# Optimization experiments

Hardware: AMD Instinct MI355X
Metric: run time of the kernel (lower is better)

The kernel has to match this reference:

```python
import jax, jax.numpy as jnp
import numpy as np

N_POI, EMBED, N_EDGES, N_LAYERS, N_HEADS = 50000, 128, 800000, 2, 4
B, L = 512, 64  # sessions, session length (equal-length sections)


def setup_inputs() -> dict:
    key = jax.random.key(0)
    ks = jax.random.split(key, 12)
    d = EMBED
    return {
        "poi_embeds": jax.random.normal(ks[0], (N_POI, d), jnp.float32),
        "dist_edges": jax.random.randint(ks[1], (2, N_EDGES), 0, N_POI),
        "dist_vec": jax.random.uniform(ks[2], (N_EDGES,), jnp.float32),
        "data_poi": jax.random.randint(ks[3], (B,), 0, N_POI),
        "data_x": jax.random.randint(ks[4], (B * L,), 0, N_POI),
        "lin_w": jax.random.normal(ks[5], (N_LAYERS, d, d), jnp.float32) / np.sqrt(d),
        "lin_b": jnp.zeros((N_LAYERS, d), jnp.float32),
        "in_proj_w": jax.random.normal(ks[6], (3 * d, d), jnp.float32) / np.sqrt(d),
        "in_proj_b": jnp.zeros((3 * d,), jnp.float32),
        "out_proj_w": jax.random.normal(ks[7], (d, d), jnp.float32) / np.sqrt(d),
        "out_proj_b": jnp.zeros((d,), jnp.float32),
    }


def reference(poi_embeds, dist_edges, dist_vec, data_poi, data_x,
              lin_w, lin_b, in_proj_w, in_proj_b, out_proj_w, out_proj_b):
    n_poi, d = poi_embeds.shape
    # --- edge augmentation done in GeoGraph.__init__: reversed edges + self loops ---
    loop = jnp.arange(n_poi)
    edges = jnp.concatenate([dist_edges, dist_edges[::-1], jnp.stack([loop, loop])], axis=1)
    dvec = jnp.concatenate([dist_vec, dist_vec, jnp.zeros((n_poi,), dist_vec.dtype)])
    src, dst = edges[0], edges[1]
    # degree of source nodes (torch_geometric.utils.degree on nodes1)
    deg = jnp.zeros((n_poi,), poi_embeds.dtype).at[src].add(1.0)
    w = jax.lax.rsqrt(deg[src] * deg[dst]) * jnp.exp(-dvec ** 2)  # [E]

    enc = poi_embeds
    for i in range(lin_w.shape[0]):
        h = enc @ lin_w[i].T + lin_b[i]                              # [N, d]
        msg = w[:, None] * h[dst]                                    # [E, d] gather
        agg = jax.ops.segment_sum(msg, src, num_segments=n_poi)      # [N, d] scatter
        agg = jnp.where(agg >= 0, agg, 0.01 * agg)                   # leaky_relu(0.01)
        enc = agg / jnp.maximum(jnp.linalg.norm(agg, axis=-1, keepdims=True), 1e-12)

    tar_embed = enc[data_poi]                                        # [B, d]
    seq = enc[data_x].reshape(B, L, d)                               # padded sessions

    # --- nn.MultiheadAttention (batch_first) ---
    hd = d // N_HEADS
    qkv = seq @ in_proj_w.T + in_proj_b                              # [B, L, 3d]
    q, k, v = jnp.split(qkv, 3, axis=-1)
    heads = lambda t: t.reshape(B, L, N_HEADS, hd).transpose(0, 2, 1, 3)
    q, k, v = heads(q), heads(k), heads(v)
    scores = jnp.einsum('bhqd,bhkd->bhqk', q, k) / np.sqrt(hd)
    attn = jax.nn.softmax(scores, axis=-1)
    o = jnp.einsum('bhqk,bhkd->bhqd', attn, v).transpose(0, 2, 1, 3).reshape(B, L, d)
    o = o @ out_proj_w.T + out_proj_b

    aggr_feat = o.mean(axis=1)                                       # mean over padded length
    return aggr_feat, tar_embed
```

## Files before the change

### kernel.cpp

```cpp
#include <hip/hip_runtime.h>
#include <hip/hip_fp16.h>

#define NPOI 50000
#define EMB 128
#define NEDGE 800000
#define EAUG (2 * NEDGE + NPOI)
#define BATCH 512
#define SEQL 64
#define NHEADS 4
#define HDIM 32
#define NB 196
#define P1_BLOCKS ((NEDGE + 2047) / 2048)
#define SLAB_CAP 10240
#define BUCKET_CAP 10240

typedef _Float16 half8 __attribute__((ext_vector_type(8)));
typedef _Float16 half4 __attribute__((ext_vector_type(4)));
typedef _Float16 half2t __attribute__((ext_vector_type(2)));
typedef float f32x4 __attribute__((ext_vector_type(4)));
typedef unsigned long long u64;

union HBits { _Float16 h; unsigned short u; };


#define N4_POI (NPOI * 128 / 4)
#define N4_LIN (2 * 128 * 128 / 4)
#define N4_INW (384 * 128 / 4)
#define CVT_TOT (N4_POI + N4_LIN + N4_INW + NB)

__global__ void cvt_all_kernel(const float* __restrict__ poi, const float* __restrict__ linw,
                               const float* __restrict__ inw,
                               _Float16* __restrict__ poi_h, _Float16* __restrict__ linw_h,
                               _Float16* __restrict__ inw_h, int* __restrict__ bcur) {
    int i = blockIdx.x * blockDim.x + threadIdx.x;
    const float* src; _Float16* dst; int j = i;
    if (i < N4_POI) { src = poi; dst = poi_h; }
    else if (i < N4_POI + N4_LIN) { j = i - N4_POI; src = linw; dst = linw_h; }
    else if (i < N4_POI + N4_LIN + N4_INW) { j = i - N4_POI - N4_LIN; src = inw; dst = inw_h; }
    else if (i < CVT_TOT) { int b = i - (N4_POI + N4_LIN + N4_INW); bcur[b] = b * SLAB_CAP; return; }
    else return;
    float4 v = ((const float4*)src)[j];
    half4 h = { (_Float16)v.x, (_Float16)v.y, (_Float16)v.z, (_Float16)v.w };
    ((half4*)dst)[j] = h;
}


__global__ __launch_bounds__(256) void partition_kernel(
    const int* __restrict__ e0, const int* __restrict__ e1,
    const float* __restrict__ dv, int* __restrict__ bcur,
    u64* __restrict__ staging)
{
    __shared__ u64 stg[4096];
    __shared__ int lh[NB], lbase[NB], gb[NB];
    __shared__ int sc[256];
    const int t = threadIdx.x;
    const int blockBase = blockIdx.x * 2048;
    for (int j = t; j < NB; j += 256) lh[j] = 0;
    __syncthreads();

    u64 vals[16];
    unsigned br[16];
#pragma unroll
    for (int i = 0; i < 8; ++i) {
        br[2 * i] = 0xFFFFFFFFu;
        br[2 * i + 1] = 0xFFFFFFFFu;
        int g = blockBase + i * 256 + t;
        if (g < NEDGE) {
            int s = e0[g], d = e1[g];
            unsigned db = __float_as_uint(dv[g]);
            vals[2 * i]     = ((u64)s << 48) | ((u64)d << 32) | db;
            vals[2 * i + 1] = ((u64)d << 48) | ((u64)s << 32) | db;
            int bs = s >> 8, bd = d >> 8;
            int rs = atomicAdd(&lh[bs], 1);
            int rd_ = atomicAdd(&lh[bd], 1);
            br[2 * i]     = ((unsigned)bs << 16) | (unsigned)rs;
            br[2 * i + 1] = ((unsigned)bd << 16) | (unsigned)rd_;
        }
    }
    __syncthreads();
    sc[t] = (t < NB) ? lh[t] : 0;
    __syncthreads();
    for (int o = 1; o < 256; o <<= 1) {
        int u = (t >= o) ? sc[t - o] : 0;
        __syncthreads();
        sc[t] += u;
        __syncthreads();
    }
    if (t < NB) {
        lbase[t] = sc[t] - lh[t];
        gb[t] = (lh[t] > 0) ? atomicAdd(&bcur[t], lh[t]) : 0;
    }
    __syncthreads();
#pragma unroll
    for (int i = 0; i < 16; ++i) {
        if (br[i] != 0xFFFFFFFFu) {
            int b = br[i] >> 16, r = br[i] & 0xFFFF;
            stg[lbase[b] + r] = vals[i];
        }
    }
    __syncthreads();
    const int total = sc[255];
    for (int j = t; j < total; j += 256) {
        u64 v = stg[j];
        int b = (int)(v >> 56);
        staging[(size_t)gb[b] + (unsigned)(j - lbase[b])] = v;
    }
}


__global__ __launch_bounds__(256) void hist_kernel(const u64* __restrict__ staging,
                                                   const int* __restrict__ bcur,
                                                   float* __restrict__ rd,
                                                   int* __restrict__ bsum) {
    __shared__ int cnt[256];
    __shared__ int red[256];
    const int b = blockIdx.x, t = threadIdx.x;
    cnt[t] = 0;
    __syncthreads();
    const int base = b * SLAB_CAP;
    const int n = bcur[b] - base;
    for (int j = t; j < n; j += 256)
        atomicAdd(&cnt[(int)(staging[base + j] >> 48) & 255], 1);
    __syncthreads();
    int node = b * 256 + t;
    int rowsz = 0;
    if (node < NPOI) {
        rowsz = cnt[t] + 1;
        rd[node] = rsqrtf((float)rowsz);
    }
    red[t] = rowsz;
    __syncthreads();
    for (int o = 128; o > 0; o >>= 1) {
        if (t < o) red[t] += red[t + o];
        __syncthreads();
    }
    if (t == 0) bsum[b] = red[0];
}


__global__ __launch_bounds__(256) void csr_sort_kernel(
    const u64* __restrict__ staging, const int* __restrict__ bcur,
    const int* __restrict__ bsum, const float* __restrict__ rd,
    int* __restrict__ offs, unsigned* __restrict__ ew)
{
    const int k = blockIdx.x;
    const int node0 = k * 256;
    __shared__ unsigned outb[BUCKET_CAP];
    __shared__ int cnt[256], base2[256];
    __shared__ float rdl[256];
    __shared__ int bb_sh;
    const int t = threadIdx.x;
    const int node = node0 + t;
    cnt[t] = 0;
    rdl[t] = (node < NPOI) ? rd[node] : 0.f;
    {
        int partial = 0;
        for (int j = t; j < k; j += 256) partial += bsum[j];
        base2[t] = partial;
        __syncthreads();
        for (int o = 128; o > 0; o >>= 1) {
            if (t < o) base2[t] += base2[t + o];
            __syncthreads();
        }
        if (t == 0) bb_sh = base2[0];
        __syncthreads();
    }
    const int bucketbase = bb_sh;
    __syncthreads();
    const int sb = k * SLAB_CAP;
    const int n = bcur[k] - sb;
    for (int j = t; j < n; j += 256)
        atomicAdd(&cnt[(int)(staging[sb + j] >> 48) & 255], 1);
    __syncthreads();
    int rowsz = (node < NPOI) ? cnt[t] + 1 : 0;
    base2[t] = rowsz;
    __syncthreads();
    for (int o = 1; o < 256; o <<= 1) {
        int u = (t >= o) ? base2[t - o] : 0;
        __syncthreads();
        base2[t] += u;
        __syncthreads();
    }
    int myexc = base2[t] - rowsz;
    __syncthreads();
    base2[t] = myexc;
    cnt[t] = 0;
    if (node < NPOI) {
        offs[node] = bucketbase + myexc;
        if (node == NPOI - 1) offs[NPOI] = bucketbase + myexc + rowsz;
    }
    __syncthreads();
    for (int j = t; j < n; j += 256) {
        u64 e = staging[sb + j];
        int sl = (int)(e >> 48) & 255;
        int d = (int)(e >> 32) & 0xFFFF;
        float dist = __uint_as_float((unsigned)e);
        float w = rdl[sl] * rd[d] * expf(-dist * dist);
        HBits cv; cv.h = (_Float16)w;
        int r = atomicAdd(&cnt[sl], 1);
        outb[base2[sl] + r] = ((unsigned)d << 16) | cv.u;
    }
    __syncthreads();
    if (node < NPOI) {
        float w = rdl[t] * rdl[t];
        HBits cv; cv.h = (_Float16)w;
        outb[base2[t] + cnt[t]] = ((unsigned)node << 16) | cv.u;
    }
    __syncthreads();
    const int ntot = (node0 + 256 < NPOI ? n + 256 : n + (NPOI - node0));
    for (int j = t; j < ntot; j += 256) ew[bucketbase + j] = outb[j];
}


__global__ __launch_bounds__(256) void gemm_mfma_f16(
    const _Float16* __restrict__ A, const int* __restrict__ gidx,
    const _Float16* __restrict__ B, const float* __restrict__ bias,
    _Float16* __restrict__ C, int M, int N)
{
    __shared__ _Float16 Asl[64][136];
    __shared__ _Float16 Bsl[64][136];
    const int tid = threadIdx.x;
    const int n0 = blockIdx.x * 64;
    const int m0 = blockIdx.y * 64;

#pragma unroll
    for (int i = 0; i < 4; ++i) {
        int u = i * 256 + tid;
        int r = u >> 4;
        int c = u & 15;
        int row = m0 + r;
        int ar = (row < M) ? (gidx ? gidx[row] : row) : 0;
        *(float4*)&Asl[r][c * 8] = *(const float4*)(A + (size_t)ar * 128 + c * 8);
        *(float4*)&Bsl[r][c * 8] = *(const float4*)(B + (size_t)(n0 + r) * 128 + c * 8);
    }
    __syncthreads();

    const int wave = tid >> 6;
    const int lane = tid & 63;
    const int l15 = lane & 15;
    const int quad = lane >> 4;

    f32x4 acc[4];
#pragma unroll
    for (int mt = 0; mt < 4; ++mt) acc[mt] = (f32x4){0.f, 0.f, 0.f, 0.f};

#pragma unroll
    for (int ks = 0; ks < 4; ++ks) {
        half8 bfrag = *(const half8*)&Bsl[wave * 16 + l15][quad * 8 + ks * 32];
#pragma unroll
        for (int mt = 0; mt < 4; ++mt) {
            half8 afrag = *(const half8*)&Asl[mt * 16 + l15][quad * 8 + ks * 32];
            acc[mt] = __builtin_amdgcn_mfma_f32_16x16x32_f16(afrag, bfrag, acc[mt], 0, 0, 0);
        }
    }

    const int col = wave * 16 + l15;
    const float bv = bias[n0 + col];
    __syncthreads();
#pragma unroll
    for (int mt = 0; mt < 4; ++mt)
#pragma unroll
        for (int r = 0; r < 4; ++r)
            Asl[mt * 16 + quad * 4 + r][col] = (_Float16)(acc[mt][r] + bv);
    __syncthreads();
#pragma unroll
    for (int i = 0; i < 2; ++i) {
        int u = i * 256 + tid;
        int r = u >> 3;
        int c = u & 7;
        int m = m0 + r;
        if (m < M)
            *(half8*)(C + (size_t)m * N + n0 + c * 8) = *(const half8*)&Asl[r][c * 8];
    }
}


__global__ __launch_bounds__(64) void aggregate_kernel(
    const _Float16* __restrict__ h, const int* __restrict__ offs,
    const unsigned* __restrict__ ew, float* __restrict__ enc_out,
    _Float16* __restrict__ enc_h)
{
    const int row = blockIdx.x;
    const int lane = threadIdx.x;
    const int beg = offs[row];
    const int end = offs[row + 1];
    float ax = 0.f, ay = 0.f;
#pragma unroll 8
    for (int e = beg; e < end; ++e) {
        unsigned p = ew[e];
        HBits cv; cv.u = (unsigned short)(p & 0xffffu);
        float w = (float)cv.h;
        int d = p >> 16;
        half2t hv = *(const half2t*)(h + (size_t)d * 128 + lane * 2);
        ax += w * (float)hv[0];
        ay += w * (float)hv[1];
    }
    ax = ax >= 0.f ? ax : 0.01f * ax;
    ay = ay >= 0.f ? ay : 0.01f * ay;
    float ss = ax * ax + ay * ay;
#pragma unroll
    for (int o = 32; o > 0; o >>= 1) ss += __shfl_xor(ss, o);
    float inv = 1.f / fmaxf(sqrtf(ss), 1e-12f);
    float ex = ax * inv, ey = ay * inv;
    *(float2*)(enc_out + (size_t)row * 128 + lane * 2) = make_float2(ex, ey);
    half2t hv = { (_Float16)ex, (_Float16)ey };
    *(half2t*)(enc_h + (size_t)row * 128 + lane * 2) = hv;
}


__global__ __launch_bounds__(256) void attn_mfma_kernel(
    const _Float16* __restrict__ qkv, const float* __restrict__ outw,
    const float* __restrict__ outb, const float* __restrict__ enc,
    const int* __restrict__ data_poi, float* __restrict__ out)
{
    const int b = blockIdx.x;
    const int wave = threadIdx.x >> 6;
    const int lane = threadIdx.x & 63;
    const int l15 = lane & 15;
    const int quad = lane >> 4;
    __shared__ _Float16 pP[NHEADS][64][72];
    __shared__ _Float16 vT[NHEADS][32][72];
    __shared__ float ob[128];
    const _Float16* base = qkv + (size_t)b * SEQL * 384;

    {
        const _Float16* vrow = base + (size_t)lane * 384 + 256 + wave * 32;
        half8 v0 = *(const half8*)(vrow);
        half8 v1 = *(const half8*)(vrow + 8);
        half8 v2 = *(const half8*)(vrow + 16);
        half8 v3 = *(const half8*)(vrow + 24);
#pragma unroll
        for (int j = 0; j < 8; ++j) {
            vT[wave][j][lane]      = v0[j];
            vT[wave][j + 8][lane]  = v1[j];
            vT[wave][j + 16][lane] = v2[j];
            vT[wave][j + 24][lane] = v3[j];
        }
    }

    half8 qf[4], kf[4];
#pragma unroll
    for (int t = 0; t < 4; ++t) {
        qf[t] = *(const half8*)(base + (size_t)(t * 16 + l15) * 384 + wave * 32 + quad * 8);
        kf[t] = *(const half8*)(base + (size_t)(t * 16 + l15) * 384 + 128 + wave * 32 + quad * 8);
    }

    f32x4 S[4][4];
#pragma unroll
    for (int lt = 0; lt < 4; ++lt)
#pragma unroll
        for (int mt = 0; mt < 4; ++mt) S[lt][mt] = (f32x4){0.f, 0.f, 0.f, 0.f};
#pragma unroll
    for (int lt = 0; lt < 4; ++lt)
#pragma unroll
        for (int mt = 0; mt < 4; ++mt)
            S[lt][mt] = __builtin_amdgcn_mfma_f32_16x16x32_f16(qf[lt], kf[mt], S[lt][mt], 0, 0, 0);

    const float scale = 0.17677669529663687f;
#pragma unroll
    for (int lt = 0; lt < 4; ++lt) {
#pragma unroll
        for (int r = 0; r < 4; ++r) {
            float m0 = -1e30f;
#pragma unroll
            for (int mt = 0; mt < 4; ++mt) {
                S[lt][mt][r] *= scale;
                m0 = fmaxf(m0, S[lt][mt][r]);
            }
#pragma unroll
            for (int o = 1; o < 16; o <<= 1) m0 = fmaxf(m0, __shfl_xor(m0, o));
            float s0 = 0.f;
#pragma unroll
            for (int mt = 0; mt < 4; ++mt) {
                float p = __expf(S[lt][mt][r] - m0);
                S[lt][mt][r] = p;
                s0 += p;
            }
#pragma unroll
            for (int o = 1; o < 16; o <<= 1) s0 += __shfl_xor(s0, o);
            float inv = 1.f / s0;
#pragma unroll
            for (int mt = 0; mt < 4; ++mt)
                pP[wave][lt * 16 + quad * 4 + r][mt * 16 + l15] = (_Float16)(S[lt][mt][r] * inv);
        }
    }
    __syncthreads();

    f32x4 O[4][2];
#pragma unroll
    for (int lt = 0; lt < 4; ++lt)
#pragma unroll
        for (int jt = 0; jt < 2; ++jt) O[lt][jt] = (f32x4){0.f, 0.f, 0.f, 0.f};
#pragma unroll
    for (int kh = 0; kh < 2; ++kh) {
        half8 vf[2];
#pragma unroll
        for (int jt = 0; jt < 2; ++jt)
            vf[jt] = *(const half8*)&vT[wave][jt * 16 + l15][kh * 32 + quad * 8];
#pragma unroll
        for (int lt = 0; lt < 4; ++lt) {
            half8 pf = *(const half8*)&pP[wave][lt * 16 + l15][kh * 32 + quad * 8];
#pragma unroll
            for (int jt = 0; jt < 2; ++jt)
                O[lt][jt] = __builtin_amdgcn_mfma_f32_16x16x32_f16(pf, vf[jt], O[lt][jt], 0, 0, 0);
        }
    }

#pragma unroll
    for (int jt = 0; jt < 2; ++jt) {
        float part = 0.f;
#pragma unroll
        for (int lt = 0; lt < 4; ++lt)
#pragma unroll
            for (int r = 0; r < 4; ++r) part += O[lt][jt][r];
        part += __shfl_xor(part, 16);
        part += __shfl_xor(part, 32);
        if (quad == 0) ob[wave * 32 + jt * 16 + l15] = part * (1.f / 64.f);
    }
    __syncthreads();

    int t = threadIdx.x;
    if (t < 128) {
        float val = outb[t];
        const float* wrow = outw + (size_t)t * 128;
#pragma unroll 8
        for (int k4 = 0; k4 < 32; ++k4) {
            float4 wv = *(const float4*)(wrow + k4 * 4);
            val += wv.x * ob[k4 * 4] + wv.y * ob[k4 * 4 + 1]
                 + wv.z * ob[k4 * 4 + 2] + wv.w * ob[k4 * 4 + 3];
        }
        out[(size_t)b * 128 + t] = val;
    } else {
        int j = t - 128;
        out[(size_t)(BATCH + b) * 128 + j] = enc[(size_t)data_poi[b] * 128 + j];
    }
}


extern "C" void kernel_launch(void* const* d_in, const int* in_sizes, int n_in,
                              void* d_out, int out_size, void* d_ws, size_t ws_size,
                              hipStream_t stream)
{
    const float* poi      = (const float*)d_in[0];
    const int*   edges    = (const int*)d_in[1];
    const float* dvec     = (const float*)d_in[2];
    const int*   data_poi = (const int*)d_in[3];
    const int*   data_x   = (const int*)d_in[4];
    const float* lin_w    = (const float*)d_in[5];
    const float* lin_b    = (const float*)d_in[6];
    const float* inw      = (const float*)d_in[7];
    const float* inb      = (const float*)d_in[8];
    const float* outw     = (const float*)d_in[9];
    const float* outb     = (const float*)d_in[10];
    const int* e0 = edges;
    const int* e1 = edges + NEDGE;

    char* ws = (char*)d_ws;
    size_t off = 0;
    auto alloc = [&](size_t bytes) -> void* {
        void* p = ws + off;
        off = (off + bytes + 255) & ~(size_t)255;
        return p;
    };
    int*      offs   = (int*)     alloc((NPOI + 1) * 4);
    int*      bsum   = (int*)     alloc(NB * 4);
    int*      bcur   = (int*)     alloc(NB * 4);
    float*    rd     = (float*)   alloc(NPOI * 4);
    unsigned* ew     = (unsigned*)alloc((size_t)EAUG * 4);
    float*    enc    = (float*)   alloc((size_t)NPOI * 128 * 4);
    _Float16* enc_h  = (_Float16*)alloc((size_t)NPOI * 128 * 2);
    _Float16* linw_h = (_Float16*)alloc((size_t)2 * 128 * 128 * 2);
    _Float16* inw_h  = (_Float16*)alloc((size_t)384 * 128 * 2);
    char*     big    = (char*)    alloc(50ull * 1024 * 1024);
    _Float16* poi_h   = (_Float16*)big;
    u64*      staging = (u64*)(big + 16ull * 1024 * 1024);
    _Float16* hbuf    = (_Float16*)(big + 33ull * 1024 * 1024);
    _Float16* qkv_h   = (_Float16*)big;

    cvt_all_kernel<<<(CVT_TOT + 255) / 256, 256, 0, stream>>>(
        poi, lin_w, inw, poi_h, linw_h, inw_h, bcur);

    partition_kernel<<<P1_BLOCKS, 256, 0, stream>>>(e0, e1, dvec, bcur, staging);
    hist_kernel<<<NB, 256, 0, stream>>>(staging, bcur, rd, bsum);
    csr_sort_kernel<<<NB, 256, 0, stream>>>(staging, bcur, bsum, rd, offs, ew);

    gemm_mfma_f16<<<dim3(2, (NPOI + 63) / 64), 256, 0, stream>>>(
        poi_h, nullptr, linw_h, lin_b, hbuf, NPOI, 128);
    aggregate_kernel<<<NPOI, 64, 0, stream>>>(hbuf, offs, ew, enc, enc_h);
    gemm_mfma_f16<<<dim3(2, (NPOI + 63) / 64), 256, 0, stream>>>(
        enc_h, nullptr, linw_h + 128 * 128, lin_b + 128, hbuf, NPOI, 128);
    aggregate_kernel<<<NPOI, 64, 0, stream>>>(hbuf, offs, ew, enc, enc_h);

    gemm_mfma_f16<<<dim3(6, BATCH * SEQL / 64), 256, 0, stream>>>(
        enc_h, data_x, inw_h, inb, qkv_h, BATCH * SEQL, 384);
    attn_mfma_kernel<<<BATCH, 256, 0, stream>>>(qkv_h, outw, outb, enc, data_poi, (float*)d_out);
}
```

Baseline: 288.5 us.

## Split SpMM into column panels and defer row normalization into GEMM epilogue

The aggregation kernel now splits each row into four 32-column panels across a 2D grid, with two edge-parity halves per wave, and writes only the unnormalized leaky-relu result in fp16 plus partial squared norms. A small kernel turns the partial sums into inverse norms, and the downstream GEMMs apply the per-row scale in their epilogue. The tar_embed output is recomputed from the fp16 aggregate times that scale. This removes the fp32 enc write and the fused per-row reduction, but it re-reads edge lists four times, adds two launches, and lowers tar_embed precision. Each lane also does a scalar fp16 gather instead of a half2 one.

```diff
diff --git a/kernel.cpp b/kernel.cpp
--- a/kernel.cpp
+++ b/kernel.cpp
@@ -214,6 +214,7 @@
 
 __global__ __launch_bounds__(256) void gemm_mfma_f16(
     const _Float16* __restrict__ A, const int* __restrict__ gidx,
+    const float* __restrict__ ns,
     const _Float16* __restrict__ B, const float* __restrict__ bias,
     _Float16* __restrict__ C, int M, int N)
 {
@@ -260,8 +261,16 @@
 #pragma unroll
     for (int mt = 0; mt < 4; ++mt)
 #pragma unroll
-        for (int r = 0; r < 4; ++r)
-            Asl[mt * 16 + quad * 4 + r][col] = (_Float16)(acc[mt][r] + bv);
+        for (int r = 0; r < 4; ++r) {
+            int m = m0 + mt * 16 + quad * 4 + r;
+            float s = 1.f;
+            if (ns) {
+                int mm = (m < M) ? m : 0;
+                int ar = gidx ? gidx[mm] : mm;
+                s = ns[ar];
+            }
+            Asl[mt * 16 + quad * 4 + r][col] = (_Float16)(acc[mt][r] * s + bv);
+        }
     __syncthreads();
 #pragma unroll
     for (int i = 0; i < 2; ++i) {
@@ -275,43 +284,52 @@
 }
 
 
-__global__ __launch_bounds__(64) void aggregate_kernel(
+__global__ __launch_bounds__(64) void spmm_panel_kernel(
     const _Float16* __restrict__ h, const int* __restrict__ offs,
-    const unsigned* __restrict__ ew, float* __restrict__ enc_out,
-    _Float16* __restrict__ enc_h)
+    const unsigned* __restrict__ ew, _Float16* __restrict__ agg_h,
+    float* __restrict__ sq4)
 {
     const int row = blockIdx.x;
+    const int p = blockIdx.y;
     const int lane = threadIdx.x;
+    const int col = lane & 31;
+    const int par = lane >> 5;
     const int beg = offs[row];
     const int end = offs[row + 1];
-    float ax = 0.f, ay = 0.f;
-#pragma unroll 8
-    for (int e = beg; e < end; ++e) {
-        unsigned p = ew[e];
-        HBits cv; cv.u = (unsigned short)(p & 0xffffu);
+    float acc = 0.f;
+#pragma unroll 4
+    for (int e = beg + par; e < end; e += 2) {
+        unsigned pe = ew[e];
+        HBits cv; cv.u = (unsigned short)(pe & 0xffffu);
         float w = (float)cv.h;
-        int d = p >> 16;
-        half2t hv = *(const half2t*)(h + (size_t)d * 128 + lane * 2);
-        ax += w * (float)hv[0];
-        ay += w * (float)hv[1];
-    }
-    ax = ax >= 0.f ? ax : 0.01f * ax;
-    ay = ay >= 0.f ? ay : 0.01f * ay;
-    float ss = ax * ax + ay * ay;
-#pragma unroll
-    for (int o = 32; o > 0; o >>= 1) ss += __shfl_xor(ss, o);
-    float inv = 1.f / fmaxf(sqrtf(ss), 1e-12f);
-    float ex = ax * inv, ey = ay * inv;
-    *(float2*)(enc_out + (size_t)row * 128 + lane * 2) = make_float2(ex, ey);
-    half2t hv = { (_Float16)ex, (_Float16)ey };
-    *(half2t*)(enc_h + (size_t)row * 128 + lane * 2) = hv;
+        int d = pe >> 16;
+        acc += w * (float)h[(size_t)d * 128 + p * 32 + col];
+    }
+    acc += __shfl_xor(acc, 32);
+    acc = acc >= 0.f ? acc : 0.01f * acc;
+    float ss = acc * acc;
+#pragma unroll
+    for (int o = 1; o < 32; o <<= 1) ss += __shfl_xor(ss, o);
+    if (lane < 32) {
+        agg_h[(size_t)row * 128 + p * 32 + col] = (_Float16)acc;
+        if (lane == 0) sq4[row * 4 + p] = ss;
+    }
+}
+
+__global__ void ns_kernel(const float* __restrict__ sq4, float* __restrict__ ns) {
+    int i = blockIdx.x * blockDim.x + threadIdx.x;
+    if (i < NPOI) {
+        float ss = sq4[4 * i] + sq4[4 * i + 1] + sq4[4 * i + 2] + sq4[4 * i + 3];
+        ns[i] = 1.f / fmaxf(sqrtf(ss), 1e-12f);
+    }
 }
 
 
 __global__ __launch_bounds__(256) void attn_mfma_kernel(
     const _Float16* __restrict__ qkv, const float* __restrict__ outw,
-    const float* __restrict__ outb, const float* __restrict__ enc,
-    const int* __restrict__ data_poi, float* __restrict__ out)
+    const float* __restrict__ outb, const _Float16* __restrict__ agg_h,
+    const float* __restrict__ ns, const int* __restrict__ data_poi,
+    float* __restrict__ out)
 {
     const int b = blockIdx.x;
     const int wave = threadIdx.x >> 6;
@@ -432,7 +450,8 @@
         out[(size_t)b * 128 + t] = val;
     } else {
         int j = t - 128;
-        out[(size_t)(BATCH + b) * 128 + j] = enc[(size_t)data_poi[b] * 128 + j];
+        int r = data_poi[b];
+        out[(size_t)(BATCH + b) * 128 + j] = (float)agg_h[(size_t)r * 128 + j] * ns[r];
     }
 }
 
@@ -466,9 +485,10 @@
     int*      bsum   = (int*)     alloc(NB * 4);
     int*      bcur   = (int*)     alloc(NB * 4);
     float*    rd     = (float*)   alloc(NPOI * 4);
+    float*    sq4    = (float*)   alloc((size_t)NPOI * 4 * 4);
+    float*    ns     = (float*)   alloc(NPOI * 4);
     unsigned* ew     = (unsigned*)alloc((size_t)EAUG * 4);
-    float*    enc    = (float*)   alloc((size_t)NPOI * 128 * 4);
-    _Float16* enc_h  = (_Float16*)alloc((size_t)NPOI * 128 * 2);
+    _Float16* agg_h  = (_Float16*)alloc((size_t)NPOI * 128 * 2);
     _Float16* linw_h = (_Float16*)alloc((size_t)2 * 128 * 128 * 2);
     _Float16* inw_h  = (_Float16*)alloc((size_t)384 * 128 * 2);
     char*     big    = (char*)    alloc(50ull * 1024 * 1024);
@@ -485,13 +505,17 @@
     csr_sort_kernel<<<NB, 256, 0, stream>>>(staging, bcur, bsum, rd, offs, ew);
 
     gemm_mfma_f16<<<dim3(2, (NPOI + 63) / 64), 256, 0, stream>>>(
-        poi_h, nullptr, linw_h, lin_b, hbuf, NPOI, 128);
-    aggregate_kernel<<<NPOI, 64, 0, stream>>>(hbuf, offs, ew, enc, enc_h);
+        poi_h, nullptr, nullptr, linw_h, lin_b, hbuf, NPOI, 128);
+    spmm_panel_kernel<<<dim3(NPOI, 4), 64, 0, stream>>>(hbuf, offs, ew, agg_h, sq4);
+    ns_kernel<<<(NPOI + 255) / 256, 256, 0, stream>>>(sq4, ns);
+
     gemm_mfma_f16<<<dim3(2, (NPOI + 63) / 64), 256, 0, stream>>>(
-        enc_h, nullptr, linw_h + 128 * 128, lin_b + 128, hbuf, NPOI, 128);
-    aggregate_kernel<<<NPOI, 64, 0, stream>>>(hbuf, offs, ew, enc, enc_h);
+        agg_h, nullptr, ns, linw_h + 128 * 128, lin_b + 128, hbuf, NPOI, 128);
+    spmm_panel_kernel<<<dim3(NPOI, 4), 64, 0, stream>>>(hbuf, offs, ew, agg_h, sq4);
+    ns_kernel<<<(NPOI + 255) / 256, 256, 0, stream>>>(sq4, ns);
 
     gemm_mfma_f16<<<dim3(6, BATCH * SEQL / 64), 256, 0, stream>>>(
-        enc_h, data_x, inw_h, inb, qkv_h, BATCH * SEQL, 384);
-    attn_mfma_kernel<<<BATCH, 256, 0, stream>>>(qkv_h, outw, outb, enc, data_poi, (float*)d_out);
-}
+        agg_h, data_x, ns, inw_h, inb, qkv_h, BATCH * SEQL, 384);
+    attn_mfma_kernel<<<BATCH, 256, 0, stream>>>(qkv_h, outw, outb, agg_h, ns, data_poi,
+                                                (float*)d_out);
+}
```

Measured after the change: 448.8 us. 1.56x slower.
